# Kernel tuning notes

Hardware: AMD Instinct MI355X
Metric: run time of the kernel (lower is better)

## Reference

```python
import jax, jax.numpy as jnp
import numpy as np

P = 3            # spline degree per axis (cubic)
NC = 64          # control points per axis
DOUT = 3         # output dimension of control points
NQ = 1_000_000   # number of query points


def open_uniform_knots(n, p):
    interior = np.linspace(0.0, 1.0, n - p + 1)
    return np.concatenate([np.zeros(p), interior, np.ones(p)]).astype(np.float32)  # len n+p+1


def bspline_basis(t, p, x):
    """Cox-de Boor basis. t:[n+p+1], x:[N] -> (i:[N,p+1] int, b:[N,p+1] float)."""
    n_basis = t.shape[0] - p - 1
    t_clamped = jnp.clip(x, t[p], t[-p - 1])
    k = jnp.searchsorted(t, t_clamped, side='right') - 1
    k = jnp.clip(k, p, n_basis - 1)                       # [N]
    i = k[:, None] + jnp.arange(-p, 1)                    # [N, p+1] global basis idx
    d = jnp.broadcast_to(jnp.eye(p + 1, dtype=x.dtype), (x.shape[0], p + 1, p + 1))
    for r in range(1, p + 1):
        j = jnp.arange(p, r - 1, -1)                      # [p-r+1]
        jk = j[None, :] + k[:, None]                      # [N, p-r+1]
        left = t[jk - p]
        right = t[jk + 1 - r]
        alpha = ((x[:, None] - left) / (right - left))[..., None]  # [N, p-r+1, 1]
        d = d.at[:, j].set((1.0 - alpha) * d[:, j - 1] + alpha * d[:, j])
    return i, d[:, p]                                     # basis values sum to 1


def setup_inputs() -> dict:
    key = jax.random.key(0)
    kq, kc = jax.random.split(key)
    queries = jax.random.uniform(kq, (NQ, 3), dtype=jnp.float32)
    control_points = jax.random.normal(kc, (NC * NC * NC, DOUT), dtype=jnp.float32)
    t = jnp.asarray(open_uniform_knots(NC, P))
    return {"queries": queries, "control_points": control_points,
            "tx": t, "ty": t, "tz": t}


def reference(queries, control_points, tx, ty, tz):
    px = py = pz = P
    ix, bx = bspline_basis(tx, px, queries[:, 0])   # [N,px+1]
    iy, by = bspline_basis(ty, py, queries[:, 1])
    iz, bz = bspline_basis(tz, pz, queries[:, 2])
    nx = tx.shape[0] - px - 1
    ny = ty.shape[0] - py - 1
    # flat index into [nx*ny*nz] control grid: ix + nx*(iy + ny*iz)
    flat_idx = (ix[:, :, None, None]
                + nx * (iy[:, None, :, None] + ny * iz[:, None, None, :]))  # [N,px+1,py+1,pz+1]
    cp_sel = control_points[flat_idx]                   # [N,px+1,py+1,pz+1,DOUT]
    y = jnp.einsum('na,nb,nc,nabcd->nd', bx, by, bz, cp_sel)
    return y
```

## Files before the change

### kernel.cpp

```cpp
#include <hip/hip_runtime.h>


#define NC 64
#define NSEG 61
#define NCELLS 512
#define WDIM 11
#define CAP 2560
#define CHUNK 512
#define NCHUNK 5
#define CHUNK_S 2048
#define OVF_CAP 4096

typedef float vfloat4 __attribute__((ext_vector_type(4)));

__device__ __forceinline__ float rcpf(float x) {
#if __has_builtin(__builtin_amdgcn_rcpf)
  return __builtin_amdgcn_rcpf(x);
#else
  return 1.0f / x;
#endif
}

__device__ __forceinline__ int span_of(float x) {
  float xc = fminf(fmaxf(x, 0.0f), 1.0f);
  int j = (int)floorf(xc * (float)NSEG);
  return j > NSEG - 1 ? NSEG - 1 : (j < 0 ? 0 : j);
}

__device__ __forceinline__ float knotv(int i) {
  float v = (float)(i - 3) * (1.0f / (float)NSEG);
  return fminf(fmaxf(v, 0.0f), 1.0f);
}

__device__ __forceinline__ void basis4(float x, int j, float N[4]) {
  float xc = fminf(fmaxf(x, 0.0f), 1.0f);
  int k = j + 3;
  float left[4], right[4];
  N[0] = 1.0f;
#pragma unroll
  for (int jj = 1; jj <= 3; ++jj) {
    left[jj] = xc - knotv(k + 1 - jj);
    right[jj] = knotv(k + jj) - xc;
    float saved = 0.0f;
#pragma unroll
    for (int r = 0; r < jj; ++r) {
      float temp = N[r] * rcpf(right[r + 1] + left[jj - r]);
      N[r] = saved + right[r + 1] * temp;
      saved = left[jj - r] * temp;
    }
    N[jj] = saved;
  }
}

__device__ __forceinline__ void eval_point(float x, float y, float z, int jx,
                                           int jy, int jz,
                                           const float* __restrict__ cp,
                                           float o[3]) {
  float Nx[4], Ny[4], Nz[4];
  basis4(x, jx, Nx);
  basis4(y, jy, Ny);
  basis4(z, jz, Nz);
  float ax = 0, ay = 0, az = 0;
#pragma unroll 1
  for (int c = 0; c < 4; ++c) {
#pragma unroll
    for (int b = 0; b < 4; ++b) {
      float w = Ny[b] * Nz[c];
      const float* row = cp + 3 * (size_t)(jx + NC * (jy + b + NC * (jz + c)));
      vfloat4 f0, f1, f2;
      __builtin_memcpy(&f0, row + 0, 16);
      __builtin_memcpy(&f1, row + 4, 16);
      __builtin_memcpy(&f2, row + 8, 16);
      ax += w * (Nx[0] * f0.x + Nx[1] * f0.w + Nx[2] * f1.z + Nx[3] * f2.y);
      ay += w * (Nx[0] * f0.y + Nx[1] * f1.x + Nx[2] * f1.w + Nx[3] * f2.z);
      az += w * (Nx[0] * f0.z + Nx[1] * f1.y + Nx[2] * f2.x + Nx[3] * f2.w);
    }
  }
  o[0] = ax; o[1] = ay; o[2] = az;
}

__device__ __forceinline__ void scan512_excl(int* arr) {
  int tid = threadIdx.x;
  int c0 = arr[tid], c1 = arr[tid + 256];
#pragma unroll
  for (int off = 1; off < 512; off <<= 1) {
    int t0 = (tid >= off) ? arr[tid - off] : 0;
    int t1 = ((tid + 256) >= off) ? arr[tid + 256 - off] : 0;
    __syncthreads();
    arr[tid] += t0;
    arr[tid + 256] += t1;
    __syncthreads();
  }
  arr[tid] -= c0;
  arr[tid + 256] -= c1;
  __syncthreads();
}


__global__ __launch_bounds__(256) void scatter_capped(
    const float* __restrict__ q, int* __restrict__ gcursor,
    int* __restrict__ ovfcnt, float4* __restrict__ ovf,
    float4* __restrict__ sorted, int nq) {
  __shared__ int hist[NCELLS];
  __shared__ int gb[NCELLS];
  __shared__ int lcur[NCELLS];
  __shared__ float4 stage[CHUNK_S];
  __shared__ int addr[CHUNK_S];
  int b = blockIdx.x, tid = threadIdx.x;
  for (int c = tid; c < NCELLS; c += 256) { hist[c] = 0; lcur[c] = 0; }
  __syncthreads();

  int s = b * CHUNK_S, e = min(nq, s + CHUNK_S);
  int nblk = e - s;
  float xs[8], ys[8], zs[8];
  int cells[8];
  unsigned us[8];
#pragma unroll
  for (int it = 0; it < 8; ++it) {
    int i = s + it * 256 + tid;
    cells[it] = -1;
    if (i < e) {
      float xyz[3];
      __builtin_memcpy(xyz, q + 3 * (size_t)i, 12);
      xs[it] = xyz[0]; ys[it] = xyz[1]; zs[it] = xyz[2];
      int jx = span_of(xyz[0]), jy = span_of(xyz[1]), jz = span_of(xyz[2]);
      cells[it] = (jx >> 3) + 8 * (jy >> 3) + 64 * (jz >> 3);
      us[it] = (unsigned)i | ((unsigned)(jx & 7) << 20) |
               ((unsigned)(jy & 7) << 23) | ((unsigned)(jz & 7) << 26);
      atomicAdd(&hist[cells[it]], 1);
    }
  }
  __syncthreads();
  int n0 = hist[tid], n1 = hist[tid + 256];
  gb[tid] = n0 ? atomicAdd(&gcursor[tid], n0) : 0;
  gb[tid + 256] = n1 ? atomicAdd(&gcursor[tid + 256], n1) : 0;
  __syncthreads();
  scan512_excl(hist);
#pragma unroll
  for (int it = 0; it < 8; ++it) {
    int cell = cells[it];
    if (cell < 0) continue;
    int rank = atomicAdd(&lcur[cell], 1);
    int rloc = hist[cell] + rank;
    int rg = gb[cell] + rank;
    if (rg < CAP) {
      stage[rloc] = make_float4(xs[it], ys[it], zs[it],
                                __int_as_float((int)us[it]));
      addr[rloc] = cell * CAP + rg;
    } else {
      addr[rloc] = -1;
      int p = atomicAdd(ovfcnt, 1);
      if (p < OVF_CAP)
        ovf[p] = make_float4(xs[it], ys[it], zs[it],
                             __int_as_float((int)(us[it] & 0xFFFFFu)));
    }
  }
  __syncthreads();
  for (int j = tid; j < nblk; j += 256) {
    int a = addr[j];
    if (a >= 0) sorted[a] = stage[j];
  }
}


__global__ __launch_bounds__(256) void eval_kernel(
    const float4* __restrict__ sorted, const int* __restrict__ cellcnt,
    const float* __restrict__ cp, float* __restrict__ out) {
  int cid = blockIdx.x / NCHUNK;
  int chunkid = blockIdx.x % NCHUNK;
  int cnt = min(cellcnt[cid], CAP);
  int q0 = chunkid * CHUNK;
  if (q0 >= cnt) return;
  int n = min(cnt - q0, CHUNK);
  size_t base = (size_t)cid * CAP + q0;
  int ox = (cid & 7) * 8, oy = ((cid >> 3) & 7) * 8, oz = (cid >> 6) * 8;
  int tid = threadIdx.x;

  __shared__ float4 lds[WDIM * WDIM * WDIM];
  __shared__ int bins[CHUNK];
  __shared__ unsigned short order[CHUNK];
  for (int e2 = tid; e2 < WDIM * WDIM * WDIM; e2 += 256) {
    int lx = e2 % WDIM, t = e2 / WDIM;
    int ly = t % WDIM, lz = t / WDIM;
    int gx = min(ox + lx, NC - 1), gy = min(oy + ly, NC - 1),
        gz = min(oz + lz, NC - 1);
    const float* p = cp + 3 * (size_t)(gx + NC * (gy + NC * gz));
    lds[e2] = make_float4(p[0], p[1], p[2], 0.0f);
  }
  bins[tid] = 0;
  bins[tid + 256] = 0;
  int k0 = -1, k1 = -1, r0 = 0, r1 = 0;
  if (tid < n)
    k0 = (int)(((unsigned)__float_as_int(sorted[base + tid].w) >> 20) & 511u);
  if (tid + 256 < n)
    k1 = (int)(((unsigned)__float_as_int(sorted[base + tid + 256].w) >> 20) & 511u);
  __syncthreads();
  if (k0 >= 0) r0 = atomicAdd(&bins[k0], 1);
  if (k1 >= 0) r1 = atomicAdd(&bins[k1], 1);
  __syncthreads();
  scan512_excl(bins);
  if (k0 >= 0) order[bins[k0] + r0] = (unsigned short)tid;
  if (k1 >= 0) order[bins[k1] + r1] = (unsigned short)(tid + 256);
  __syncthreads();

  for (int t2 = tid; t2 < n; t2 += 256) {
    int lidx = order[t2];
    float4 s = sorted[base + lidx];
    unsigned u = (unsigned)__float_as_int(s.w);
    int oi = (int)(u & 0xFFFFFu);
    int lx0 = (int)((u >> 20) & 7), ly0 = (int)((u >> 23) & 7),
        lz0 = (int)((u >> 26) & 7);
    float Nx[4], Ny[4], Nz[4];
    basis4(s.x, ox + lx0, Nx);
    basis4(s.y, oy + ly0, Ny);
    basis4(s.z, oz + lz0, Nz);

    float ax = 0.0f, ay = 0.0f, az = 0.0f;
#pragma unroll
    for (int c = 0; c < 4; ++c) {
#pragma unroll
      for (int b = 0; b < 4; ++b) {
        float w = Ny[b] * Nz[c];
        const float4* row = &lds[((lz0 + c) * WDIM + (ly0 + b)) * WDIM + lx0];
        float4 p0 = row[0], p1 = row[1], p2 = row[2], p3 = row[3];
        ax += w * (Nx[0] * p0.x + Nx[1] * p1.x + Nx[2] * p2.x + Nx[3] * p3.x);
        ay += w * (Nx[0] * p0.y + Nx[1] * p1.y + Nx[2] * p2.y + Nx[3] * p3.y);
        az += w * (Nx[0] * p0.z + Nx[1] * p1.z + Nx[2] * p2.z + Nx[3] * p3.z);
      }
    }
    float o[3] = {ax, ay, az};
    __builtin_memcpy(out + 3 * (size_t)oi, o, 12);
  }
}

__global__ __launch_bounds__(256) void ovf_kernel(const float4* __restrict__ ovf,
                                                  const int* __restrict__ ovfcnt,
                                                  const float* __restrict__ cp,
                                                  float* __restrict__ out) {
  int n = min(*ovfcnt, OVF_CAP);
  for (int i = blockIdx.x * 256 + threadIdx.x; i < n; i += gridDim.x * 256) {
    float4 s = ovf[i];
    int oi = __float_as_int(s.w);
    float o[3];
    eval_point(s.x, s.y, s.z, span_of(s.x), span_of(s.y), span_of(s.z), cp, o);
    __builtin_memcpy(out + 3 * (size_t)oi, o, 12);
  }
}

__global__ __launch_bounds__(256) void spline_direct_kernel(
    const float* __restrict__ q, const float* __restrict__ cp,
    float* __restrict__ out, int nq) {
  int i = blockIdx.x * 256 + threadIdx.x;
  if (i >= nq) return;
  float xyz[3];
  __builtin_memcpy(xyz, q + 3 * (size_t)i, 12);
  float o[3];
  eval_point(xyz[0], xyz[1], xyz[2], span_of(xyz[0]), span_of(xyz[1]),
             span_of(xyz[2]), cp, o);
  __builtin_memcpy(out + 3 * (size_t)i, o, 12);
}

extern "C" void kernel_launch(void* const* d_in, const int* in_sizes, int n_in,
                              void* d_out, int out_size, void* d_ws,
                              size_t ws_size, hipStream_t stream) {
  const float* queries = (const float*)d_in[0];
  const float* control = (const float*)d_in[1];
  float* out = (float*)d_out;
  int nq = in_sizes[0] / 3;

  size_t meta = (NCELLS + 1) * sizeof(int);
  size_t metap = (meta + 15) & ~15ull;
  size_t need = metap + (size_t)OVF_CAP * 16 + (size_t)NCELLS * CAP * 16;

  if (nq <= (1 << 20) && ws_size >= need) {
    int* gcursor = (int*)d_ws;
    int* ovfcnt = gcursor + NCELLS;
    float4* ovf = (float4*)((char*)d_ws + metap);
    float4* sorted = ovf + OVF_CAP;
    hipMemsetAsync(d_ws, 0, meta, stream);
    int nb = (nq + CHUNK_S - 1) / CHUNK_S;
    scatter_capped<<<nb, 256, 0, stream>>>(queries, gcursor, ovfcnt, ovf,
                                           sorted, nq);
    eval_kernel<<<NCELLS * NCHUNK, 256, 0, stream>>>(sorted, gcursor, control,
                                                     out);
    ovf_kernel<<<4, 256, 0, stream>>>(ovf, ovfcnt, control, out);
  } else {
    spline_direct_kernel<<<(nq + 255) / 256, 256, 0, stream>>>(queries, control,
                                                               out, nq);
  }
}
```

Measured before the change: 135.5 us.

## Use persistent eval blocks with an atomic work queue and 512-thread blocks

The eval kernel becomes persistent: a fixed grid of 512-thread blocks pulls (cell, chunk) work items from a global atomic counter instead of launching one block per item, and each chunk grows to 1024 points. The scatter kernel also moves to 512 threads, so the 512-entry scan uses one element per thread. The aim is to cut launch and tail imbalance from empty or uneven cells and to reduce scan work per thread. In exchange, the control-point window is reloaded into LDS for every item, extra barriers are added per item, and larger blocks may lower occupancy.

```diff
diff --git a/kernel.cpp b/kernel.cpp
--- a/kernel.cpp
+++ b/kernel.cpp
@@ -6,8 +6,10 @@
 #define NCELLS 512
 #define WDIM 11
 #define CAP 2560
-#define CHUNK 512
-#define NCHUNK 5
+#define CHUNK 1024
+#define NCHUNK 3
+#define NITEMS (NCELLS * NCHUNK)
+#define EVAL_BLOCKS 1024
 #define CHUNK_S 2048
 #define OVF_CAP 4096
 
@@ -81,23 +83,20 @@
 
 __device__ __forceinline__ void scan512_excl(int* arr) {
   int tid = threadIdx.x;
-  int c0 = arr[tid], c1 = arr[tid + 256];
+  int c = arr[tid];
 #pragma unroll
   for (int off = 1; off < 512; off <<= 1) {
-    int t0 = (tid >= off) ? arr[tid - off] : 0;
-    int t1 = ((tid + 256) >= off) ? arr[tid + 256 - off] : 0;
-    __syncthreads();
-    arr[tid] += t0;
-    arr[tid + 256] += t1;
-    __syncthreads();
-  }
-  arr[tid] -= c0;
-  arr[tid + 256] -= c1;
-  __syncthreads();
-}
-
-
-__global__ __launch_bounds__(256) void scatter_capped(
+    int t = (tid >= off) ? arr[tid - off] : 0;
+    __syncthreads();
+    arr[tid] += t;
+    __syncthreads();
+  }
+  arr[tid] -= c;
+  __syncthreads();
+}
+
+
+__global__ __launch_bounds__(512) void scatter_capped(
     const float* __restrict__ q, int* __restrict__ gcursor,
     int* __restrict__ ovfcnt, float4* __restrict__ ovf,
     float4* __restrict__ sorted, int nq) {
@@ -107,17 +106,18 @@
   __shared__ float4 stage[CHUNK_S];
   __shared__ int addr[CHUNK_S];
   int b = blockIdx.x, tid = threadIdx.x;
-  for (int c = tid; c < NCELLS; c += 256) { hist[c] = 0; lcur[c] = 0; }
+  hist[tid] = 0;
+  lcur[tid] = 0;
   __syncthreads();
 
   int s = b * CHUNK_S, e = min(nq, s + CHUNK_S);
   int nblk = e - s;
-  float xs[8], ys[8], zs[8];
-  int cells[8];
-  unsigned us[8];
-#pragma unroll
-  for (int it = 0; it < 8; ++it) {
-    int i = s + it * 256 + tid;
+  float xs[4], ys[4], zs[4];
+  int cells[4];
+  unsigned us[4];
+#pragma unroll
+  for (int it = 0; it < 4; ++it) {
+    int i = s + it * 512 + tid;
     cells[it] = -1;
     if (i < e) {
       float xyz[3];
@@ -131,13 +131,12 @@
     }
   }
   __syncthreads();
-  int n0 = hist[tid], n1 = hist[tid + 256];
+  int n0 = hist[tid];
   gb[tid] = n0 ? atomicAdd(&gcursor[tid], n0) : 0;
-  gb[tid + 256] = n1 ? atomicAdd(&gcursor[tid + 256], n1) : 0;
   __syncthreads();
   scan512_excl(hist);
 #pragma unroll
-  for (int it = 0; it < 8; ++it) {
+  for (int it = 0; it < 4; ++it) {
     int cell = cells[it];
     if (cell < 0) continue;
     int rank = atomicAdd(&lcur[cell], 1);
@@ -156,80 +155,90 @@
     }
   }
   __syncthreads();
-  for (int j = tid; j < nblk; j += 256) {
+  for (int j = tid; j < nblk; j += 512) {
     int a = addr[j];
     if (a >= 0) sorted[a] = stage[j];
   }
 }
 
 
-__global__ __launch_bounds__(256) void eval_kernel(
+__global__ __launch_bounds__(512) void eval_kernel(
     const float4* __restrict__ sorted, const int* __restrict__ cellcnt,
-    const float* __restrict__ cp, float* __restrict__ out) {
-  int cid = blockIdx.x / NCHUNK;
-  int chunkid = blockIdx.x % NCHUNK;
-  int cnt = min(cellcnt[cid], CAP);
-  int q0 = chunkid * CHUNK;
-  if (q0 >= cnt) return;
-  int n = min(cnt - q0, CHUNK);
-  size_t base = (size_t)cid * CAP + q0;
-  int ox = (cid & 7) * 8, oy = ((cid >> 3) & 7) * 8, oz = (cid >> 6) * 8;
+    const float* __restrict__ cp, float* __restrict__ out,
+    int* __restrict__ qhead) {
+  __shared__ float4 lds[WDIM * WDIM * WDIM];
+  __shared__ int bins[NCELLS];
+  __shared__ unsigned short order[CHUNK];
+  __shared__ int s_item;
   int tid = threadIdx.x;
 
-  __shared__ float4 lds[WDIM * WDIM * WDIM];
-  __shared__ int bins[CHUNK];
-  __shared__ unsigned short order[CHUNK];
-  for (int e2 = tid; e2 < WDIM * WDIM * WDIM; e2 += 256) {
-    int lx = e2 % WDIM, t = e2 / WDIM;
-    int ly = t % WDIM, lz = t / WDIM;
-    int gx = min(ox + lx, NC - 1), gy = min(oy + ly, NC - 1),
-        gz = min(oz + lz, NC - 1);
-    const float* p = cp + 3 * (size_t)(gx + NC * (gy + NC * gz));
-    lds[e2] = make_float4(p[0], p[1], p[2], 0.0f);
-  }
-  bins[tid] = 0;
-  bins[tid + 256] = 0;
-  int k0 = -1, k1 = -1, r0 = 0, r1 = 0;
-  if (tid < n)
-    k0 = (int)(((unsigned)__float_as_int(sorted[base + tid].w) >> 20) & 511u);
-  if (tid + 256 < n)
-    k1 = (int)(((unsigned)__float_as_int(sorted[base + tid + 256].w) >> 20) & 511u);
-  __syncthreads();
-  if (k0 >= 0) r0 = atomicAdd(&bins[k0], 1);
-  if (k1 >= 0) r1 = atomicAdd(&bins[k1], 1);
-  __syncthreads();
-  scan512_excl(bins);
-  if (k0 >= 0) order[bins[k0] + r0] = (unsigned short)tid;
-  if (k1 >= 0) order[bins[k1] + r1] = (unsigned short)(tid + 256);
-  __syncthreads();
-
-  for (int t2 = tid; t2 < n; t2 += 256) {
-    int lidx = order[t2];
-    float4 s = sorted[base + lidx];
-    unsigned u = (unsigned)__float_as_int(s.w);
-    int oi = (int)(u & 0xFFFFFu);
-    int lx0 = (int)((u >> 20) & 7), ly0 = (int)((u >> 23) & 7),
-        lz0 = (int)((u >> 26) & 7);
-    float Nx[4], Ny[4], Nz[4];
-    basis4(s.x, ox + lx0, Nx);
-    basis4(s.y, oy + ly0, Ny);
-    basis4(s.z, oz + lz0, Nz);
-
-    float ax = 0.0f, ay = 0.0f, az = 0.0f;
-#pragma unroll
-    for (int c = 0; c < 4; ++c) {
-#pragma unroll
-      for (int b = 0; b < 4; ++b) {
-        float w = Ny[b] * Nz[c];
-        const float4* row = &lds[((lz0 + c) * WDIM + (ly0 + b)) * WDIM + lx0];
-        float4 p0 = row[0], p1 = row[1], p2 = row[2], p3 = row[3];
-        ax += w * (Nx[0] * p0.x + Nx[1] * p1.x + Nx[2] * p2.x + Nx[3] * p3.x);
-        ay += w * (Nx[0] * p0.y + Nx[1] * p1.y + Nx[2] * p2.y + Nx[3] * p3.y);
-        az += w * (Nx[0] * p0.z + Nx[1] * p1.z + Nx[2] * p2.z + Nx[3] * p3.z);
+  for (;;) {
+    __syncthreads();
+    if (tid == 0) s_item = atomicAdd(qhead, 1);
+    __syncthreads();
+    int item = s_item;
+    if (item >= NITEMS) break;
+    int chunkid = item >> 9;
+    int cid = item & (NCELLS - 1);
+    int cnt = min(cellcnt[cid], CAP);
+    int q0 = chunkid * CHUNK;
+    if (q0 >= cnt) continue;
+    int n = min(cnt - q0, CHUNK);
+    size_t base = (size_t)cid * CAP + q0;
+    int ox = (cid & 7) * 8, oy = ((cid >> 3) & 7) * 8, oz = (cid >> 6) * 8;
+
+    for (int e2 = tid; e2 < WDIM * WDIM * WDIM; e2 += 512) {
+      int lx = e2 % WDIM, t = e2 / WDIM;
+      int ly = t % WDIM, lz = t / WDIM;
+      int gx = min(ox + lx, NC - 1), gy = min(oy + ly, NC - 1),
+          gz = min(oz + lz, NC - 1);
+      const float* p = cp + 3 * (size_t)(gx + NC * (gy + NC * gz));
+      lds[e2] = make_float4(p[0], p[1], p[2], 0.0f);
+    }
+    bins[tid] = 0;
+    int k0 = -1, k1 = -1, r0 = 0, r1 = 0;
+    if (tid < n)
+      k0 = (int)(((unsigned)__float_as_int(sorted[base + tid].w) >> 20) & 511u);
+    if (tid + 512 < n)
+      k1 = (int)(((unsigned)__float_as_int(sorted[base + tid + 512].w) >> 20) &
+                 511u);
+    __syncthreads();
+    if (k0 >= 0) r0 = atomicAdd(&bins[k0], 1);
+    if (k1 >= 0) r1 = atomicAdd(&bins[k1], 1);
+    __syncthreads();
+    scan512_excl(bins);
+    if (k0 >= 0) order[bins[k0] + r0] = (unsigned short)tid;
+    if (k1 >= 0) order[bins[k1] + r1] = (unsigned short)(tid + 512);
+    __syncthreads();
+
+    for (int t2 = tid; t2 < n; t2 += 512) {
+      int lidx = order[t2];
+      float4 s = sorted[base + lidx];
+      unsigned u = (unsigned)__float_as_int(s.w);
+      int oi = (int)(u & 0xFFFFFu);
+      int lx0 = (int)((u >> 20) & 7), ly0 = (int)((u >> 23) & 7),
+          lz0 = (int)((u >> 26) & 7);
+      float Nx[4], Ny[4], Nz[4];
+      basis4(s.x, ox + lx0, Nx);
+      basis4(s.y, oy + ly0, Ny);
+      basis4(s.z, oz + lz0, Nz);
+
+      float ax = 0.0f, ay = 0.0f, az = 0.0f;
+#pragma unroll
+      for (int c = 0; c < 4; ++c) {
+#pragma unroll
+        for (int b = 0; b < 4; ++b) {
+          float w = Ny[b] * Nz[c];
+          const float4* row = &lds[((lz0 + c) * WDIM + (ly0 + b)) * WDIM + lx0];
+          float4 p0 = row[0], p1 = row[1], p2 = row[2], p3 = row[3];
+          ax += w * (Nx[0] * p0.x + Nx[1] * p1.x + Nx[2] * p2.x + Nx[3] * p3.x);
+          ay += w * (Nx[0] * p0.y + Nx[1] * p1.y + Nx[2] * p2.y + Nx[3] * p3.y);
+          az += w * (Nx[0] * p0.z + Nx[1] * p1.z + Nx[2] * p2.z + Nx[3] * p3.z);
+        }
       }
-    }
-    float o[3] = {ax, ay, az};
-    __builtin_memcpy(out + 3 * (size_t)oi, o, 12);
+      float o[3] = {ax, ay, az};
+      __builtin_memcpy(out + 3 * (size_t)oi, o, 12);
+    }
   }
 }
 
@@ -268,21 +277,22 @@
   float* out = (float*)d_out;
   int nq = in_sizes[0] / 3;
 
-  size_t meta = (NCELLS + 1) * sizeof(int);
+  size_t meta = (NCELLS + 2) * sizeof(int);
   size_t metap = (meta + 15) & ~15ull;
   size_t need = metap + (size_t)OVF_CAP * 16 + (size_t)NCELLS * CAP * 16;
 
   if (nq <= (1 << 20) && ws_size >= need) {
     int* gcursor = (int*)d_ws;
     int* ovfcnt = gcursor + NCELLS;
+    int* qhead = gcursor + NCELLS + 1;
     float4* ovf = (float4*)((char*)d_ws + metap);
     float4* sorted = ovf + OVF_CAP;
     hipMemsetAsync(d_ws, 0, meta, stream);
     int nb = (nq + CHUNK_S - 1) / CHUNK_S;
-    scatter_capped<<<nb, 256, 0, stream>>>(queries, gcursor, ovfcnt, ovf,
+    scatter_capped<<<nb, 512, 0, stream>>>(queries, gcursor, ovfcnt, ovf,
                                            sorted, nq);
-    eval_kernel<<<NCELLS * NCHUNK, 256, 0, stream>>>(sorted, gcursor, control,
-                                                     out);
+    eval_kernel<<<EVAL_BLOCKS, 512, 0, stream>>>(sorted, gcursor, control, out,
+                                                 qhead);
     ovf_kernel<<<4, 256, 0, stream>>>(ovf, ovfcnt, control, out);
   } else {
     spline_direct_kernel<<<(nq + 255) / 256, 256, 0, stream>>>(queries, control,
```

After: 134.8 us. Within noise of the previous version (-0.5%).
